# Performance work log

Measured on AMD Instinct MI355X. Metric: run time of the kernel, lower is better.

The kernel has to match this reference:

```python
import jax, jax.numpy as jnp
import numpy as np

# dims matching init_kwargs / input_specs
N, C, H, W = 8, 256, 64, 64
OUT_C, KH, KW = 256, 3, 3
STRIDE, PAD = 1, 1
OUT_H = (H - KH + 2 * PAD) // STRIDE + 1  # 64
OUT_W = (W - KW + 2 * PAD) // STRIDE + 1  # 64
K = KH * KW


def setup_inputs() -> dict:
    key = jax.random.key(0)
    k1, k2, k3 = jax.random.split(key, 3)
    x = jax.random.normal(k1, (N, C, H, W), dtype=jnp.float32)
    offset = jax.random.normal(k2, (N, 2 * K, OUT_H, OUT_W), dtype=jnp.float32)
    # kaiming-uniform-ish scale for weight (fan_in = C*KH*KW)
    bound = 1.0 / np.sqrt(C * KH * KW)
    weight = jax.random.uniform(k3, (OUT_C, C, KH, KW), dtype=jnp.float32,
                                minval=-bound, maxval=bound)
    return {"input": x, "offset": offset, "weight": weight}


def _deform_conv(x, offset, weight):
    # base sampling positions in pixel coords: y = oy*stride + ky - pad
    ky = jnp.repeat(jnp.arange(KH, dtype=jnp.float32) - PAD, KW)  # [K]
    kx = jnp.tile(jnp.arange(KW, dtype=jnp.float32) - PAD, KH)    # [K]
    oy = jnp.arange(OUT_H, dtype=jnp.float32) * STRIDE            # [outH]
    ox = jnp.arange(OUT_W, dtype=jnp.float32) * STRIDE            # [outW]
    base_y = ky[:, None, None] + oy[None, :, None]  # [K, outH, 1]
    base_x = kx[:, None, None] + ox[None, None, :]  # [K, 1, outW]

    off = offset.reshape(N, K, 2, OUT_H, OUT_W)
    y = base_y[None] + off[:, :, 0]  # [N, K, outH, outW], offset channel 0 = dy
    xp = base_x[None] + off[:, :, 1]  # channel 1 = dx

    # bilinear sample with zero padding (grid_sample align_corners=True, zeros)
    y0 = jnp.floor(y)
    x0 = jnp.floor(xp)
    bidx = jnp.arange(N)[:, None, None, None]
    acc = jnp.zeros((N, K, OUT_H, OUT_W, C), dtype=x.dtype)
    for dy in (0.0, 1.0):
        for dx in (0.0, 1.0):
            yi = y0 + dy
            xi = x0 + dx
            wgt = (1.0 - jnp.abs(y - yi)) * (1.0 - jnp.abs(xp - xi))
            valid = ((yi >= 0) & (yi <= H - 1) & (xi >= 0) & (xi <= W - 1))
            yc = jnp.clip(yi, 0, H - 1).astype(jnp.int32)
            xc = jnp.clip(xi, 0, W - 1).astype(jnp.int32)
            g = x[bidx, :, yc, xc]  # [N, K, outH, outW, C]
            acc = acc + g * (wgt * valid.astype(x.dtype))[..., None]

    # weight.view(outC, -1) flattens (C, KH, KW) -> (C, K) ordering
    w = weight.reshape(OUT_C, C, K)
    out = jnp.einsum('nkhwc,ock->nohw', acc, w)  # [N, outC, outH, outW]
    return out


def reference(input, offset, weight):
    # NOTE: original forward never adds bias -> faithfully omitted
    return _deform_conv(input, offset, weight)
```

## Files before the change

kernel.cpp:

```cpp
#include <hip/hip_runtime.h>
#include <hip/hip_bf16.h>
#include <hip/hip_fp16.h>
#include <stdint.h>


typedef short short8 __attribute__((ext_vector_type(8)));
typedef float f32x4 __attribute__((ext_vector_type(4)));

__device__ __forceinline__ float bflo(uint32_t u) { return __uint_as_float(u << 16); }
__device__ __forceinline__ float bfhi(uint32_t u) { return __uint_as_float(u & 0xffff0000u); }
__device__ __forceinline__ uint32_t packbf(float a, float b) {
  unsigned short ua = __builtin_bit_cast(unsigned short, __float2bfloat16(a));
  unsigned short ub = __builtin_bit_cast(unsigned short, __float2bfloat16(b));
  return (uint32_t)ua | ((uint32_t)ub << 16);
}
__device__ __forceinline__ float h2f(uint32_t bits16) {
  __half h = __builtin_bit_cast(__half, (unsigned short)bits16);
  return __half2float(h);
}

__global__ __launch_bounds__(256) void prep_x_kernel(const float* __restrict__ x,
                                                     unsigned short* __restrict__ xb) {
  __shared__ float tile[64][65];
  int bn   = blockIdx.x >> 8;
  int rem  = blockIdx.x & 255;
  int y    = rem >> 2;
  int cblk = rem & 3;
  int tid  = threadIdx.x;
  const float* src = x + ((size_t)(bn * 256 + cblk * 64)) * 4096 + y * 64;
#pragma unroll
  for (int i = 0; i < 4; ++i) {
    int u  = i * 256 + tid;
    int cl = u >> 4;
    int xs = (u & 15) * 4;
    float4 v = *(const float4*)(src + cl * 4096 + xs);
    tile[cl][xs] = v.x; tile[cl][xs + 1] = v.y;
    tile[cl][xs + 2] = v.z; tile[cl][xs + 3] = v.w;
  }
  __syncthreads();
  unsigned short* dst = xb + ((size_t)(bn * 64 + y) * 64) * 256 + cblk * 64;
#pragma unroll
  for (int i = 0; i < 8; ++i) {
    int v2  = i * 256 + tid;
    int xc  = v2 >> 5;
    int cl2 = (v2 & 31) * 2;
    *(uint32_t*)(dst + xc * 256 + cl2) = packbf(tile[cl2][xc], tile[cl2 + 1][xc]);
  }
}

__global__ __launch_bounds__(256) void prep_wc_kernel(const float* __restrict__ w,
                                                      const float* __restrict__ offset,
                                                      unsigned short* __restrict__ w3s,
                                                      unsigned short* __restrict__ coords) {
  if (blockIdx.x < 2304) {
    int idx = blockIdx.x * 256 + threadIdx.x;
    int t   = idx >> 14;
    int r2  = idx & 16383;
    int g   = r2 >> 3;
    int e   = r2 & 7;
    int oc  = g >> 3;
    int kk8 = (g & 7) ^ (oc & 7);
    int kk  = kk8 * 8 + e;
    int c   = (t & 3) * 64 + kk;
    int k   = t >> 2;
    w3s[idx] = __builtin_bit_cast(unsigned short, __float2bfloat16(w[(oc * 256 + c) * 9 + k]));
  } else {
    int idx = (blockIdx.x - 2304) * 256 + threadIdx.x;
    int ow  = idx & 63;
    int oh  = (idx >> 6) & 63;
    int r   = idx >> 12;
    int k   = r % 9;
    int bn  = r / 9;
    int ky = k / 3 - 1;
    int kx = k % 3 - 1;
    float offy = offset[((bn * 18 + 2 * k    ) * 64 + oh) * 64 + ow];
    float offx = offset[((bn * 18 + 2 * k + 1) * 64 + oh) * 64 + ow];
    float y = (float)(oh + ky) + offy;
    float x = (float)(ow + kx) + offx;
    float y0f = floorf(y), x0f = floorf(x);
    float fy = y - y0f, fx = x - x0f;
    int y0 = (int)y0f, x0 = (int)x0f;
    int y1 = y0 + 1, x1 = x0 + 1;
    float vy0 = (y0 >= 0 && y0 <= 63) ? 1.0f : 0.0f;
    float vy1 = (y1 >= 0 && y1 <= 63) ? 1.0f : 0.0f;
    float vx0 = (x0 >= 0 && x0 <= 63) ? 1.0f : 0.0f;
    float vx1 = (x1 >= 0 && x1 <= 63) ? 1.0f : 0.0f;
    float wy0 = (1.0f - fy) * vy0, wy1 = fy * vy1;
    float wx0 = (1.0f - fx) * vx0, wx1 = fx * vx1;
    int y0c = min(max(y0, 0), 63), y1c = min(max(y1, 0), 63);
    int x0c = min(max(x0, 0), 63), x1c = min(max(x1, 0), 63);
    unsigned short ent[8];
    ent[0] = __builtin_bit_cast(unsigned short, __float2half(wy0 * wx0));
    ent[1] = __builtin_bit_cast(unsigned short, __float2half(wy0 * wx1));
    ent[2] = __builtin_bit_cast(unsigned short, __float2half(wy1 * wx0));
    ent[3] = __builtin_bit_cast(unsigned short, __float2half(wy1 * wx1));
    ent[4] = (unsigned short)(y0c * 64 + x0c);
    ent[5] = (unsigned short)(y0c * 64 + x1c);
    ent[6] = (unsigned short)(y1c * 64 + x0c);
    ent[7] = (unsigned short)(y1c * 64 + x1c);
    *(uint4*)(coords + (size_t)idx * 8) = *(const uint4*)ent;
  }
}

__global__ __launch_bounds__(512, 4) void deform_mfma_kernel(
    const unsigned short* __restrict__ xb,
    const unsigned short* __restrict__ coords,
    const unsigned short* __restrict__ w3s,
    float* __restrict__ out) {
  __shared__ __align__(16) unsigned short At[64 * 72];
  __shared__ __align__(16) unsigned short Bt[256 * 64];

  int bn  = blockIdx.x & 7;
  int oh  = blockIdx.x >> 3;
  int tid = threadIdx.x;

  int w     = tid >> 6;
  int lane  = tid & 63;
  int wrow  = w & 1;
  int wcol  = w >> 1;
  int mrow  = lane & 15;
  int quad  = lane >> 4;

  int srow = tid >> 3;
  int sg   = tid & 7;

  const unsigned short* xbn = xb + (size_t)bn * (64 * 64 * 256);
  const char* gbase = (const char*)xbn + sg * 16;
  const unsigned short* cbase = coords + ((size_t)((bn * 9) * 64 + oh) * 64 + srow) * 8;

  f32x4 acc[2][4] = {};

#define BDMA(TT)                                                                \
  {                                                                             \
    const unsigned short* src = w3s + (TT) * 16384;                             \
    _Pragma("unroll")                                                           \
    for (int j = 0; j < 4; ++j) {                                               \
      int base16 = j * 512 + w * 64;                                            \
      __builtin_amdgcn_global_load_lds(                                         \
          (const __attribute__((address_space(1))) void*)(src + (base16 + lane) * 8), \
          (__attribute__((address_space(3))) void*)(Bt + base16 * 8),           \
          16, 0, 0);                                                            \
    }                                                                           \
  }

#define ASTAGE(TT)                                                              \
  {                                                                             \
    uint4 e = *(const uint4*)(cbase + ((TT) >> 2) * 32768);                     \
    const char* gb = gbase + ((TT) & 3) * 128;                                  \
    uint4 c00 = *(const uint4*)(gb + ((e.z & 0xffffu) << 9));                   \
    uint4 c01 = *(const uint4*)(gb + ((e.z >> 16) << 9));                       \
    uint4 c10 = *(const uint4*)(gb + ((e.w & 0xffffu) << 9));                   \
    uint4 c11 = *(const uint4*)(gb + ((e.w >> 16) << 9));                       \
    float w00 = h2f(e.x & 0xffffu), w01 = h2f(e.x >> 16);                       \
    float w10 = h2f(e.y & 0xffffu), w11 = h2f(e.y >> 16);                       \
    float a0 = bflo(c00.x) * w00 + bflo(c01.x) * w01 + bflo(c10.x) * w10 + bflo(c11.x) * w11; \
    float a1 = bfhi(c00.x) * w00 + bfhi(c01.x) * w01 + bfhi(c10.x) * w10 + bfhi(c11.x) * w11; \
    float a2 = bflo(c00.y) * w00 + bflo(c01.y) * w01 + bflo(c10.y) * w10 + bflo(c11.y) * w11; \
    float a3 = bfhi(c00.y) * w00 + bfhi(c01.y) * w01 + bfhi(c10.y) * w10 + bfhi(c11.y) * w11; \
    float a4 = bflo(c00.z) * w00 + bflo(c01.z) * w01 + bflo(c10.z) * w10 + bflo(c11.z) * w11; \
    float a5 = bfhi(c00.z) * w00 + bfhi(c01.z) * w01 + bfhi(c10.z) * w10 + bfhi(c11.z) * w11; \
    float a6 = bflo(c00.w) * w00 + bflo(c01.w) * w01 + bflo(c10.w) * w10 + bflo(c11.w) * w11; \
    float a7 = bfhi(c00.w) * w00 + bfhi(c01.w) * w01 + bfhi(c10.w) * w10 + bfhi(c11.w) * w11; \
    uint4 pk;                                                                   \
    pk.x = packbf(a0, a1); pk.y = packbf(a2, a3);                               \
    pk.z = packbf(a4, a5); pk.w = packbf(a6, a7);                               \
    *(uint4*)(&At[srow * 72 + sg * 8]) = pk;                                    \
  }

  BDMA(0)
  ASTAGE(0)
  __syncthreads();

  short8 af[2][2];
  short8 bfr[2][4];

  for (int t = 0; t < 36; ++t) {
#pragma unroll
    for (int ks = 0; ks < 2; ++ks) {
#pragma unroll
      for (int m = 0; m < 2; ++m)
        af[m][ks] = *(const short8*)(&At[(wrow * 32 + m * 16 + mrow) * 72 + ks * 32 + quad * 8]);
#pragma unroll
      for (int nn = 0; nn < 4; ++nn) {
        int oc  = wcol * 64 + nn * 16 + mrow;
        int g16 = oc * 8 + ((ks * 4 + quad) ^ (mrow & 7));
        bfr[ks][nn] = *(const short8*)(Bt + g16 * 8);
      }
    }
    __syncthreads();

    if (t < 35) {
      BDMA(t + 1)
      ASTAGE(t + 1)
    }
#pragma unroll
    for (int ks = 0; ks < 2; ++ks)
#pragma unroll
      for (int m = 0; m < 2; ++m)
#pragma unroll
        for (int nn = 0; nn < 4; ++nn)
          acc[m][nn] = __builtin_amdgcn_mfma_f32_16x16x32_bf16(af[m][ks], bfr[ks][nn], acc[m][nn], 0, 0, 0);
    __syncthreads();
  }

  float* outp = out + (size_t)(bn * 256) * 4096 + oh * 64;
#pragma unroll
  for (int m = 0; m < 2; ++m) {
    int ow0 = wrow * 32 + m * 16 + quad * 4;
#pragma unroll
    for (int nn = 0; nn < 4; ++nn) {
      int oc = wcol * 64 + nn * 16 + mrow;
      *(f32x4*)(outp + oc * 4096 + ow0) = acc[m][nn];
    }
  }
#undef BDMA
#undef ASTAGE
}

extern "C" void kernel_launch(void* const* d_in, const int* in_sizes, int n_in,
                              void* d_out, int out_size, void* d_ws, size_t ws_size,
                              hipStream_t stream) {
  (void)in_sizes; (void)n_in; (void)out_size; (void)ws_size;
  const float* x      = (const float*)d_in[0];
  const float* offset = (const float*)d_in[1];
  const float* weight = (const float*)d_in[2];
  float* out = (float*)d_out;

  unsigned short* xb     = (unsigned short*)d_ws;
  unsigned short* w3s    = xb + (size_t)8 * 64 * 64 * 256;
  unsigned short* coords = w3s + (size_t)36 * 16384;

  prep_x_kernel<<<2048, 256, 0, stream>>>(x, xb);
  prep_wc_kernel<<<3456, 256, 0, stream>>>(weight, offset, w3s, coords);
  deform_mfma_kernel<<<512, 512, 0, stream>>>(xb, coords, w3s, out);
}
```

Before: 153.3 us.

## Switch to fp16 packed bilinear math, hoist per-tap coords, merge prep kernels

Converts x and weights to fp16 instead of bf16 so bilinear interpolation can use packed half2 FMAs directly on loaded data, and uses the f16 MFMA. The per-tap coordinate/weight load is hoisted out of the channel-chunk loop, so it runs once per tap instead of four times. The two prep kernels are merged into one launch. The cost is fp16 range and precision in the interpolation accumulation, and fewer launches with extra branching in the prep kernel.

Result: no change. 152.2 us (-0.7%).

```diff
diff --git a/kernel.cpp b/kernel.cpp
--- a/kernel.cpp
+++ b/kernel.cpp
@@ -1,59 +1,57 @@
 #include <hip/hip_runtime.h>
-#include <hip/hip_bf16.h>
 #include <hip/hip_fp16.h>
 #include <stdint.h>
 
 
-typedef short short8 __attribute__((ext_vector_type(8)));
+typedef _Float16 half8 __attribute__((ext_vector_type(8)));
 typedef float f32x4 __attribute__((ext_vector_type(4)));
 
-__device__ __forceinline__ float bflo(uint32_t u) { return __uint_as_float(u << 16); }
-__device__ __forceinline__ float bfhi(uint32_t u) { return __uint_as_float(u & 0xffff0000u); }
-__device__ __forceinline__ uint32_t packbf(float a, float b) {
-  unsigned short ua = __builtin_bit_cast(unsigned short, __float2bfloat16(a));
-  unsigned short ub = __builtin_bit_cast(unsigned short, __float2bfloat16(b));
-  return (uint32_t)ua | ((uint32_t)ub << 16);
-}
-__device__ __forceinline__ float h2f(uint32_t bits16) {
-  __half h = __builtin_bit_cast(__half, (unsigned short)bits16);
-  return __half2float(h);
-}
-
-__global__ __launch_bounds__(256) void prep_x_kernel(const float* __restrict__ x,
-                                                     unsigned short* __restrict__ xb) {
+__device__ __forceinline__ __half2 h2(uint32_t u) {
+  return __builtin_bit_cast(__half2, u);
+}
+__device__ __forceinline__ uint32_t packh2f(float a, float b) {
+  return __builtin_bit_cast(uint32_t, __floats2half2_rn(a, b));
+}
+__device__ __forceinline__ __half2 duplo(uint32_t u) {
+  return __half2half2(__builtin_bit_cast(__half, (unsigned short)(u & 0xffffu)));
+}
+__device__ __forceinline__ __half2 duphi(uint32_t u) {
+  return __half2half2(__builtin_bit_cast(__half, (unsigned short)(u >> 16)));
+}
+
+__global__ __launch_bounds__(256) void prep_all_kernel(
+    const float* __restrict__ x, const float* __restrict__ w,
+    const float* __restrict__ offset,
+    unsigned short* __restrict__ xb, unsigned short* __restrict__ w3s,
+    unsigned short* __restrict__ coords) {
   __shared__ float tile[64][65];
-  int bn   = blockIdx.x >> 8;
-  int rem  = blockIdx.x & 255;
-  int y    = rem >> 2;
-  int cblk = rem & 3;
-  int tid  = threadIdx.x;
-  const float* src = x + ((size_t)(bn * 256 + cblk * 64)) * 4096 + y * 64;
-#pragma unroll
-  for (int i = 0; i < 4; ++i) {
-    int u  = i * 256 + tid;
-    int cl = u >> 4;
-    int xs = (u & 15) * 4;
-    float4 v = *(const float4*)(src + cl * 4096 + xs);
-    tile[cl][xs] = v.x; tile[cl][xs + 1] = v.y;
-    tile[cl][xs + 2] = v.z; tile[cl][xs + 3] = v.w;
-  }
-  __syncthreads();
-  unsigned short* dst = xb + ((size_t)(bn * 64 + y) * 64) * 256 + cblk * 64;
-#pragma unroll
-  for (int i = 0; i < 8; ++i) {
-    int v2  = i * 256 + tid;
-    int xc  = v2 >> 5;
-    int cl2 = (v2 & 31) * 2;
-    *(uint32_t*)(dst + xc * 256 + cl2) = packbf(tile[cl2][xc], tile[cl2 + 1][xc]);
-  }
-}
-
-__global__ __launch_bounds__(256) void prep_wc_kernel(const float* __restrict__ w,
-                                                      const float* __restrict__ offset,
-                                                      unsigned short* __restrict__ w3s,
-                                                      unsigned short* __restrict__ coords) {
-  if (blockIdx.x < 2304) {
-    int idx = blockIdx.x * 256 + threadIdx.x;
+  int tid = threadIdx.x;
+  if (blockIdx.x < 2048) {
+    int bn   = blockIdx.x >> 8;
+    int rem  = blockIdx.x & 255;
+    int y    = rem >> 2;
+    int cblk = rem & 3;
+    const float* src = x + ((size_t)(bn * 256 + cblk * 64)) * 4096 + y * 64;
+#pragma unroll
+    for (int i = 0; i < 4; ++i) {
+      int u  = i * 256 + tid;
+      int cl = u >> 4;
+      int xs = (u & 15) * 4;
+      float4 v = *(const float4*)(src + cl * 4096 + xs);
+      tile[cl][xs] = v.x; tile[cl][xs + 1] = v.y;
+      tile[cl][xs + 2] = v.z; tile[cl][xs + 3] = v.w;
+    }
+    __syncthreads();
+    unsigned short* dst = xb + ((size_t)(bn * 64 + y) * 64) * 256 + cblk * 64;
+#pragma unroll
+    for (int i = 0; i < 8; ++i) {
+      int v2  = i * 256 + tid;
+      int xc  = v2 >> 5;
+      int cl2 = (v2 & 31) * 2;
+      *(uint32_t*)(dst + xc * 256 + cl2) = packh2f(tile[cl2][xc], tile[cl2 + 1][xc]);
+    }
+  } else if (blockIdx.x < 4352) {
+    int idx = (blockIdx.x - 2048) * 256 + tid;
     int t   = idx >> 14;
     int r2  = idx & 16383;
     int g   = r2 >> 3;
@@ -63,9 +61,9 @@
     int kk  = kk8 * 8 + e;
     int c   = (t & 3) * 64 + kk;
     int k   = t >> 2;
-    w3s[idx] = __builtin_bit_cast(unsigned short, __float2bfloat16(w[(oc * 256 + c) * 9 + k]));
+    w3s[idx] = __builtin_bit_cast(unsigned short, __float2half(w[(oc * 256 + c) * 9 + k]));
   } else {
-    int idx = (blockIdx.x - 2304) * 256 + threadIdx.x;
+    int idx = (blockIdx.x - 4352) * 256 + tid;
     int ow  = idx & 63;
     int oh  = (idx >> 6) & 63;
     int r   = idx >> 12;
@@ -76,9 +74,9 @@
     float offy = offset[((bn * 18 + 2 * k    ) * 64 + oh) * 64 + ow];
     float offx = offset[((bn * 18 + 2 * k + 1) * 64 + oh) * 64 + ow];
     float y = (float)(oh + ky) + offy;
-    float x = (float)(ow + kx) + offx;
-    float y0f = floorf(y), x0f = floorf(x);
-    float fy = y - y0f, fx = x - x0f;
+    float x2 = (float)(ow + kx) + offx;
+    float y0f = floorf(y), x0f = floorf(x2);
+    float fy = y - y0f, fx = x2 - x0f;
     int y0 = (int)y0f, x0 = (int)x0f;
     int y1 = y0 + 1, x1 = x0 + 1;
     float vy0 = (y0 >= 0 && y0 <= 63) ? 1.0f : 0.0f;
@@ -114,12 +112,12 @@
   int oh  = blockIdx.x >> 3;
   int tid = threadIdx.x;
 
-  int w     = tid >> 6;
-  int lane  = tid & 63;
-  int wrow  = w & 1;
-  int wcol  = w >> 1;
-  int mrow  = lane & 15;
-  int quad  = lane >> 4;
+  int w    = tid >> 6;
+  int lane = tid & 63;
+  int wrow = w & 1;
+  int wcol = w >> 1;
+  int mrow = lane & 15;
+  int quad = lane >> 4;
 
   int srow = tid >> 3;
   int sg   = tid & 7;
@@ -127,6 +125,7 @@
   const unsigned short* xbn = xb + (size_t)bn * (64 * 64 * 256);
   const char* gbase = (const char*)xbn + sg * 16;
   const unsigned short* cbase = coords + ((size_t)((bn * 9) * 64 + oh) * 64 + srow) * 8;
+  unsigned short* awr = At + srow * 72 + sg * 8;
 
   f32x4 acc[2][4] = {};
 
@@ -145,62 +144,88 @@
 
 #define ASTAGE(TT)                                                              \
   {                                                                             \
-    uint4 e = *(const uint4*)(cbase + ((TT) >> 2) * 32768);                     \
-    const char* gb = gbase + ((TT) & 3) * 128;                                  \
-    uint4 c00 = *(const uint4*)(gb + ((e.z & 0xffffu) << 9));                   \
-    uint4 c01 = *(const uint4*)(gb + ((e.z >> 16) << 9));                       \
-    uint4 c10 = *(const uint4*)(gb + ((e.w & 0xffffu) << 9));                   \
-    uint4 c11 = *(const uint4*)(gb + ((e.w >> 16) << 9));                       \
-    float w00 = h2f(e.x & 0xffffu), w01 = h2f(e.x >> 16);                       \
-    float w10 = h2f(e.y & 0xffffu), w11 = h2f(e.y >> 16);                       \
-    float a0 = bflo(c00.x) * w00 + bflo(c01.x) * w01 + bflo(c10.x) * w10 + bflo(c11.x) * w11; \
-    float a1 = bfhi(c00.x) * w00 + bfhi(c01.x) * w01 + bfhi(c10.x) * w10 + bfhi(c11.x) * w11; \
-    float a2 = bflo(c00.y) * w00 + bflo(c01.y) * w01 + bflo(c10.y) * w10 + bflo(c11.y) * w11; \
-    float a3 = bfhi(c00.y) * w00 + bfhi(c01.y) * w01 + bfhi(c10.y) * w10 + bfhi(c11.y) * w11; \
-    float a4 = bflo(c00.z) * w00 + bflo(c01.z) * w01 + bflo(c10.z) * w10 + bflo(c11.z) * w11; \
-    float a5 = bfhi(c00.z) * w00 + bfhi(c01.z) * w01 + bfhi(c10.z) * w10 + bfhi(c11.z) * w11; \
-    float a6 = bflo(c00.w) * w00 + bflo(c01.w) * w01 + bflo(c10.w) * w10 + bflo(c11.w) * w11; \
-    float a7 = bfhi(c00.w) * w00 + bfhi(c01.w) * w01 + bfhi(c10.w) * w10 + bfhi(c11.w) * w11; \
+    uint4 c00 = *(const uint4*)(p00 + ((TT) & 3) * 128);                        \
+    uint4 c01 = *(const uint4*)(p01 + ((TT) & 3) * 128);                        \
+    uint4 c10 = *(const uint4*)(p10 + ((TT) & 3) * 128);                        \
+    uint4 c11 = *(const uint4*)(p11 + ((TT) & 3) * 128);                        \
+    __half2 r0 = __hmul2(h2(c00.x), w00);                                       \
+    r0 = __hfma2(h2(c01.x), w01, r0);                                           \
+    r0 = __hfma2(h2(c10.x), w10, r0);                                           \
+    r0 = __hfma2(h2(c11.x), w11, r0);                                           \
+    __half2 r1 = __hmul2(h2(c00.y), w00);                                       \
+    r1 = __hfma2(h2(c01.y), w01, r1);                                           \
+    r1 = __hfma2(h2(c10.y), w10, r1);                                           \
+    r1 = __hfma2(h2(c11.y), w11, r1);                                           \
+    __half2 r2 = __hmul2(h2(c00.z), w00);                                       \
+    r2 = __hfma2(h2(c01.z), w01, r2);                                           \
+    r2 = __hfma2(h2(c10.z), w10, r2);                                           \
+    r2 = __hfma2(h2(c11.z), w11, r2);                                           \
+    __half2 r3 = __hmul2(h2(c00.w), w00);                                       \
+    r3 = __hfma2(h2(c01.w), w01, r3);                                           \
+    r3 = __hfma2(h2(c10.w), w10, r3);                                           \
+    r3 = __hfma2(h2(c11.w), w11, r3);                                           \
     uint4 pk;                                                                   \
-    pk.x = packbf(a0, a1); pk.y = packbf(a2, a3);                               \
-    pk.z = packbf(a4, a5); pk.w = packbf(a6, a7);                               \
-    *(uint4*)(&At[srow * 72 + sg * 8]) = pk;                                    \
-  }
-
+    pk.x = __builtin_bit_cast(uint32_t, r0);                                    \
+    pk.y = __builtin_bit_cast(uint32_t, r1);                                    \
+    pk.z = __builtin_bit_cast(uint32_t, r2);                                    \
+    pk.w = __builtin_bit_cast(uint32_t, r3);                                    \
+    *(uint4*)awr = pk;                                                          \
+  }
+
+#define TAPSETUP(TAP)                                                           \
+  {                                                                             \
+    uint4 ce = *(const uint4*)(cbase + (TAP) * 32768);                          \
+    w00 = duplo(ce.x); w01 = duphi(ce.x);                                       \
+    w10 = duplo(ce.y); w11 = duphi(ce.y);                                       \
+    p00 = gbase + ((size_t)(ce.z & 0xffffu) << 9);                              \
+    p01 = gbase + ((size_t)(ce.z >> 16) << 9);                                  \
+    p10 = gbase + ((size_t)(ce.w & 0xffffu) << 9);                              \
+    p11 = gbase + ((size_t)(ce.w >> 16) << 9);                                  \
+  }
+
+  __half2 w00, w01, w10, w11;
+  const char *p00, *p01, *p10, *p11;
+
+  TAPSETUP(0)
   BDMA(0)
   ASTAGE(0)
   __syncthreads();
 
-  short8 af[2][2];
-  short8 bfr[2][4];
-
-  for (int t = 0; t < 36; ++t) {
-#pragma unroll
-    for (int ks = 0; ks < 2; ++ks) {
-#pragma unroll
-      for (int m = 0; m < 2; ++m)
-        af[m][ks] = *(const short8*)(&At[(wrow * 32 + m * 16 + mrow) * 72 + ks * 32 + quad * 8]);
-#pragma unroll
-      for (int nn = 0; nn < 4; ++nn) {
-        int oc  = wcol * 64 + nn * 16 + mrow;
-        int g16 = oc * 8 + ((ks * 4 + quad) ^ (mrow & 7));
-        bfr[ks][nn] = *(const short8*)(Bt + g16 * 8);
+  half8 af[2][2];
+  half8 bfr[2][4];
+
+  for (int tap = 0; tap < 9; ++tap) {
+#pragma unroll
+    for (int cc = 0; cc < 4; ++cc) {
+      const int t = tap * 4 + cc;
+#pragma unroll
+      for (int ks = 0; ks < 2; ++ks) {
+#pragma unroll
+        for (int m = 0; m < 2; ++m)
+          af[m][ks] = *(const half8*)(&At[(wrow * 32 + m * 16 + mrow) * 72 + ks * 32 + quad * 8]);
+#pragma unroll
+        for (int nn = 0; nn < 4; ++nn) {
+          int oc  = wcol * 64 + nn * 16 + mrow;
+          int g16 = oc * 8 + ((ks * 4 + quad) ^ (mrow & 7));
+          bfr[ks][nn] = *(const half8*)(&Bt[g16 * 8]);
+        }
       }
-    }
-    __syncthreads();
-
-    if (t < 35) {
-      BDMA(t + 1)
-      ASTAGE(t + 1)
-    }
-#pragma unroll
-    for (int ks = 0; ks < 2; ++ks)
-#pragma unroll
-      for (int m = 0; m < 2; ++m)
-#pragma unroll
-        for (int nn = 0; nn < 4; ++nn)
-          acc[m][nn] = __builtin_amdgcn_mfma_f32_16x16x32_bf16(af[m][ks], bfr[ks][nn], acc[m][nn], 0, 0, 0);
-    __syncthreads();
+      __syncthreads();
+
+      if (t < 35) {
+        BDMA(t + 1)
+        if (cc == 3) TAPSETUP(tap + 1)
+        ASTAGE(t + 1)
+      }
+#pragma unroll
+      for (int ks = 0; ks < 2; ++ks)
+#pragma unroll
+        for (int m = 0; m < 2; ++m)
+#pragma unroll
+          for (int nn = 0; nn < 4; ++nn)
+            acc[m][nn] = __builtin_amdgcn_mfma_f32_16x16x32_f16(af[m][ks], bfr[ks][nn], acc[m][nn], 0, 0, 0);
+      __syncthreads();
+    }
   }
 
   float* outp = out + (size_t)(bn * 256) * 4096 + oh * 64;
@@ -215,6 +240,7 @@
   }
 #undef BDMA
 #undef ASTAGE
+#undef TAPSETUP
 }
 
 extern "C" void kernel_launch(void* const* d_in, const int* in_sizes, int n_in,
@@ -230,7 +256,6 @@
   unsigned short* w3s    = xb + (size_t)8 * 64 * 64 * 256;
   unsigned short* coords = w3s + (size_t)36 * 16384;
 
-  prep_x_kernel<<<2048, 256, 0, stream>>>(x, xb);
-  prep_wc_kernel<<<3456, 256, 0, stream>>>(weight, offset, w3s, coords);
+  prep_all_kernel<<<5504, 256, 0, stream>>>(x, weight, offset, xb, w3s, coords);
   deform_mfma_kernel<<<512, 512, 0, stream>>>(xb, coords, w3s, out);
 }
```
